# Kernel tuning notes

Measured on AMD Instinct MI355X. Metric: run time of the kernel, lower is better.

The kernel has to match this reference:

```python
import jax, jax.numpy as jnp
import numpy as np


def _gru_cell(x, h, Wih, Whh, bih, bhh):
    # torch nn.GRU cell math: gates ordered [r, z, n]
    gi = Wih @ x + bih
    gh = Whh @ h + bhh
    ir, iz, inn = jnp.split(gi, 3)
    hr, hz, hn = jnp.split(gh, 3)
    r = jax.nn.sigmoid(ir + hr)
    z = jax.nn.sigmoid(iz + hz)
    n = jnp.tanh(inn + r * hn)
    return (1.0 - z) * n + z * h


def _lrelu(x):
    # torch nn.LeakyReLU default negative_slope=0.01
    return jnp.where(x >= 0, x, 0.01 * x)


def setup_inputs() -> dict:
    key = jax.random.key(0)
    ks = jax.random.split(key, 24)
    V, E, H, C, S, T = 32000, 512, 1024, 2048, 256, 129
    w = lambda k, shape: jax.random.normal(k, shape, jnp.float32) * 0.02
    return {
        "inputs": jax.random.randint(ks[0], (T,), 0, V),
        "h1": jax.random.normal(ks[1], (H,), jnp.float32),
        "h2": jax.random.normal(ks[2], (H,), jnp.float32),
        "projected_keys": jax.random.normal(ks[3], (S, H), jnp.float32),
        "encoder_outputs": jax.random.normal(ks[4], (S, C), jnp.float32),
        "embeds": jax.random.normal(ks[5], (V, E), jnp.float32),
        "Wq": w(ks[6], (H, H)),
        "v_att": w(ks[7], (H,)),
        "W_ih1": w(ks[8], (3 * H, E + C)),
        "W_hh1": w(ks[9], (3 * H, H)),
        "b_ih1": w(ks[10], (3 * H,)),
        "b_hh1": w(ks[11], (3 * H,)),
        "W_ih2": w(ks[12], (3 * H, H + C)),
        "W_hh2": w(ks[13], (3 * H, H)),
        "b_ih2": w(ks[14], (3 * H,)),
        "b_hh2": w(ks[15], (3 * H,)),
        "W_pre": w(ks[16], (H, E + H + C)),
        "b_pre": w(ks[17], (H,)),
        "W_out": w(ks[18], (E, H)),
        "b_out": w(ks[19], (E,)),
    }


def reference(inputs, h1, h2, projected_keys, encoder_outputs, embeds, Wq, v_att,
              W_ih1, W_hh1, b_ih1, b_hh1, W_ih2, W_hh2, b_ih2, b_hh2,
              W_pre, b_pre, W_out, b_out):
    # teacher_forcing = 1.0 -> decoder input at step i is inputs[i] (ground truth)
    emb_seq = embeds[inputs[:-1]]  # [T-1, E]

    def step(carry, emb):
        h1, h2 = carry
        # additive attention: query from top-layer hidden state
        q = Wq @ h2                                     # [H]
        e = jnp.tanh(projected_keys + q) @ v_att        # [S]
        alphas = jax.nn.softmax(e)                      # [S]
        context = alphas @ encoder_outputs              # [C]
        h1n = _gru_cell(jnp.concatenate([emb, context]), h1, W_ih1, W_hh1, b_ih1, b_hh1)
        o1 = _lrelu(h1n)                                # dropout identity (eval)
        h2n = _gru_cell(jnp.concatenate([o1, context]), h2, W_ih2, W_hh2, b_ih2, b_hh2)
        o2 = _lrelu(h2n)
        pre = _lrelu(W_pre @ jnp.concatenate([emb, o2, context]) + b_pre)  # [H]
        out = W_out @ o2 + b_out                        # [E]
        return (h1n, h2n), (out, pre, alphas)

    (h1f, h2f), (outs, pres, alphas) = jax.lax.scan(step, (h1, h2), emb_seq)
    # torch.cat(outputs, dim=1) of [1,1,E] pieces -> [1, T-1, E]
    return outs[None], pres[None], alphas, h1f, h2f
```

## Files before the change

kernel.cpp:

```cpp
#include <hip/hip_runtime.h>

typedef unsigned int uint32;

#define GBLK 256
#define BT 512
#define NSTEP 128

struct Params {
  const int* inputs;
  const float *h1_in, *h2_in, *embeds, *vatt;
  const float *pk, *enc, *Wq, *Wih1, *Whh1, *Wih2, *Whh2, *Wpre, *Wout;
  const float *bih1, *bhh1, *bih2, *bhh2, *bpre, *bout;
  float* out;
  float* ws;
  int* bar;
};

__device__ __forceinline__ float blo(uint32 u) { return __uint_as_float(u << 16); }
__device__ __forceinline__ float bhi(uint32 u) { return __uint_as_float(u & 0xffff0000u); }
__device__ __forceinline__ uint32 bfr(float f) {
  uint32 u = __float_as_uint(f);
  return (u + 0x7fffu + ((u >> 16) & 1u)) >> 16;
}

__device__ __forceinline__ float ald(const float* a) {
  return __hip_atomic_load(a, __ATOMIC_RELAXED, __HIP_MEMORY_SCOPE_AGENT);
}
__device__ __forceinline__ void ast(float* a, float v) {
  __hip_atomic_store(a, v, __ATOMIC_RELAXED, __HIP_MEMORY_SCOPE_AGENT);
}

__device__ __forceinline__ float wsum(float v) {
#pragma unroll
  for (int o = 32; o; o >>= 1) v += __shfl_xor(v, o, 64);
  return v;
}

__device__ __forceinline__ void ldchunk(const float* W, size_t base, int lane, uint32* r) {
  const float* wf = W + base + lane * 8;
  float4 a = *(const float4*)wf;
  float4 c = *(const float4*)(wf + 4);
  r[0] = bfr(a.x) | (bfr(a.y) << 16);
  r[1] = bfr(a.z) | (bfr(a.w) << 16);
  r[2] = bfr(c.x) | (bfr(c.y) << 16);
  r[3] = bfr(c.z) | (bfr(c.w) << 16);
}

__device__ __forceinline__ float dotchunk(const uint32* r, const float* xc, int lane) {
  const float* x = xc + lane * 8;
  float4 x0 = *(const float4*)x, x1 = *(const float4*)(x + 4);
  return blo(r[0]) * x0.x + bhi(r[0]) * x0.y + blo(r[1]) * x0.z + bhi(r[1]) * x0.w +
         blo(r[2]) * x1.x + bhi(r[2]) * x1.y + blo(r[3]) * x1.z + bhi(r[3]) * x1.w;
}

__device__ __forceinline__ void gbar(int* bar, int k) {
  __syncthreads();
  if (threadIdx.x == 0) {
    const int grp = blockIdx.x >> 4;
    int* gcnt = bar + grp * 32;
    int* grel = bar + 512 + grp * 32;
    int* rcnt = bar + 1024;
    int* rrel = bar + 1056;
    int v = __hip_atomic_fetch_add(gcnt, 1, __ATOMIC_RELEASE, __HIP_MEMORY_SCOPE_AGENT);
    if (v == k * 16 - 1) {
      int r = __hip_atomic_fetch_add(rcnt, 1, __ATOMIC_RELEASE, __HIP_MEMORY_SCOPE_AGENT);
      if (r == k * 16 - 1)
        __hip_atomic_store(rrel, k, __ATOMIC_RELAXED, __HIP_MEMORY_SCOPE_AGENT);
      while (__hip_atomic_load(rrel, __ATOMIC_RELAXED, __HIP_MEMORY_SCOPE_AGENT) < k)
        __builtin_amdgcn_s_sleep(1);
      __hip_atomic_store(grel, k, __ATOMIC_RELAXED, __HIP_MEMORY_SCOPE_AGENT);
    } else {
      while (__hip_atomic_load(grel, __ATOMIC_RELAXED, __HIP_MEMORY_SCOPE_AGENT) < k)
        __builtin_amdgcn_s_sleep(1);
    }
  }
  __syncthreads();
}

__device__ __forceinline__ float sigm(float x) { return 1.f / (1.f + expf(-x)); }
__device__ __forceinline__ float lrelu(float x) { return x >= 0.f ? x : 0.01f * x; }

__global__ __launch_bounds__(BT, 2) void dec_regw_kernel(Params p) {
  __shared__ float sx[5632];
  __shared__ float s_red[8];
  __shared__ float s_part[72];

  const int tid = threadIdx.x;
  const int lane = tid & 63;
  const int w = tid >> 6;
  const int b = blockIdx.x;
  const int gw = b * 8 + w;
  const int i0 = b * 4;
  const int j0 = b * 8;

  float* h1w = p.ws + 2048;
  float* h2w = p.ws + 3072;
  float* qw = p.ws + 4096;
  float* evw = p.ws + 5120;
  float* ctxw = p.ws + 5376;
  float* o1w = p.ws + 7424;
  float* o2w = p.ws + 8448;
  float* gh1 = p.ws + 9472;
  float* gh2 = p.ws + 12544;

  float* outs = p.out;
  float* pres = p.out + 65536;
  float* alph = p.out + 196608;
  float* h1f = p.out + 229376;
  float* h2f = p.out + 230400;

  uint32 wa[48];
  if (gw < 1024) {
#pragma unroll
    for (int c = 0; c < 7; ++c)
      ldchunk(p.Wpre, (size_t)gw * 3584 + c * 512, lane, wa + 4 * c);
    ldchunk(p.Whh1, (size_t)gw * 1024, lane, wa + 28);
    ldchunk(p.Whh1, (size_t)gw * 1024 + 512, lane, wa + 32);
    ldchunk(p.Whh1, (size_t)(gw + 1024) * 1024, lane, wa + 36);
    ldchunk(p.Whh1, (size_t)(gw + 1024) * 1024 + 512, lane, wa + 40);
    wa[44] = wa[45] = wa[46] = wa[47] = 0u;
  } else {
    const int widx = gw - 1024;
    ldchunk(p.Whh1, (size_t)(2048 + widx) * 1024, lane, wa + 0);
    ldchunk(p.Whh1, (size_t)(2048 + widx) * 1024 + 512, lane, wa + 4);
#pragma unroll
    for (int r = 0; r < 3; ++r) {
      ldchunk(p.Whh2, (size_t)(widx + r * 1024) * 1024, lane, wa + 8 + 8 * r);
      ldchunk(p.Whh2, (size_t)(widx + r * 1024) * 1024 + 512, lane, wa + 12 + 8 * r);
    }
    ldchunk(p.Wq, (size_t)widx * 1024, lane, wa + 32);
    ldchunk(p.Wq, (size_t)widx * 1024 + 512, lane, wa + 36);
    const int wr = widx & 511;
    ldchunk(p.Wout, (size_t)wr * 1024, lane, wa + 40);
    ldchunk(p.Wout, (size_t)wr * 1024 + 512, lane, wa + 44);
  }

  uint32 wd[32];
#pragma unroll
  for (int k = 0; k < 8; ++k) {
    const int mm = w + 8 * k;
    const int mmc = mm < 60 ? mm : 0;
    const int r = mmc / 15, m = mmc % 15, g = m / 5, c = m % 5;
    ldchunk(p.Wih1, (size_t)(g * 1024 + i0 + r) * 2560 + c * 512, lane, wd + 4 * k);
  }

  uint32 we9[36];
#pragma unroll
  for (int k = 0; k < 9; ++k) {
    const int mm = w + 8 * k;
    const int r = mm / 18, m = mm % 18, g = m / 6, c = m % 6;
    ldchunk(p.Wih2, (size_t)(g * 1024 + i0 + r) * 3072 + c * 512, lane, we9 + 4 * k);
  }

  uint32 wenc[4] = {0u, 0u, 0u, 0u};
  if (tid < 256) {
    const float* er = p.enc + (size_t)tid * 2048 + j0;
    float4 a = *(const float4*)er, c = *(const float4*)(er + 4);
    wenc[0] = bfr(a.x) | (bfr(a.y) << 16);
    wenc[1] = bfr(a.z) | (bfr(a.w) << 16);
    wenc[2] = bfr(c.x) | (bfr(c.y) << 16);
    wenc[3] = bfr(c.z) | (bfr(c.w) << 16);
  }

  const int d0 = tid * 2;
  const float pk0 = p.pk[(size_t)b * 1024 + d0];
  const float pk1 = p.pk[(size_t)b * 1024 + d0 + 1];
  const float va0 = p.vatt[d0];
  const float va1 = p.vatt[d0 + 1];

  if (gw < 16) ast(h1w + gw * 64 + lane, p.h1_in[gw * 64 + lane]);
  else if (gw < 32) ast(h2w + (gw - 16) * 64 + lane, p.h2_in[(gw - 16) * 64 + lane]);

  int bk = 0;
  gbar(p.bar, ++bk);

  for (int t = 0; t <= NSTEP; ++t) {
    gbar(p.bar, ++bk);
    {
      const float* embp = p.embeds + (size_t)p.inputs[t > 0 ? t - 1 : 0] * 512;
      for (int i = tid; i < 5632; i += BT) {
        float v;
        if (i < 512) v = embp[i];
        else if (i < 1536) v = ald(o2w + i - 512);
        else if (i < 3584) v = ald(ctxw + i - 1536);
        else if (i < 4608) v = ald(h1w + i - 3584);
        else v = ald(h2w + i - 4608);
        sx[i] = v;
      }
      __syncthreads();
      if (gw < 1024) {
        if (t > 0) {
          float s = 0.f;
#pragma unroll
          for (int c = 0; c < 7; ++c) s += dotchunk(wa + 4 * c, sx + 512 * c, lane);
          s = wsum(s);
          if (lane == 0) pres[(size_t)(t - 1) * 1024 + gw] = lrelu(s + p.bpre[gw]);
        }
        float s1 = dotchunk(wa + 28, sx + 3584, lane) + dotchunk(wa + 32, sx + 4096, lane);
        s1 = wsum(s1);
        if (lane == 0) ast(gh1 + gw, s1 + p.bhh1[gw]);
        float s2 = dotchunk(wa + 36, sx + 3584, lane) + dotchunk(wa + 40, sx + 4096, lane);
        s2 = wsum(s2);
        if (lane == 0) ast(gh1 + 1024 + gw, s2 + p.bhh1[1024 + gw]);
      } else {
        const int widx = gw - 1024;
        float s = dotchunk(wa + 0, sx + 3584, lane) + dotchunk(wa + 4, sx + 4096, lane);
        s = wsum(s);
        if (lane == 0) ast(gh1 + 2048 + widx, s + p.bhh1[2048 + widx]);
#pragma unroll
        for (int r = 0; r < 3; ++r) {
          float t2 = dotchunk(wa + 8 + 8 * r, sx + 4608, lane) +
                     dotchunk(wa + 12 + 8 * r, sx + 5120, lane);
          t2 = wsum(t2);
          if (lane == 0) ast(gh2 + widx + 1024 * r, t2 + p.bhh2[widx + 1024 * r]);
        }
        float sq = dotchunk(wa + 32, sx + 4608, lane) + dotchunk(wa + 36, sx + 5120, lane);
        sq = wsum(sq);
        if (lane == 0) ast(qw + widx, sq);
        if (t > 0 && widx < 512) {
          float so = dotchunk(wa + 40, sx + 512, lane) + dotchunk(wa + 44, sx + 1024, lane);
          so = wsum(so);
          if (lane == 0) outs[(size_t)(t - 1) * 512 + widx] = so + p.bout[widx];
        }
      }
    }
    if (t == NSTEP) break;

    gbar(p.bar, ++bk);
    {
      float q0 = ald(qw + d0), q1 = ald(qw + d0 + 1);
      float acc = va0 * tanhf(pk0 + q0) + va1 * tanhf(pk1 + q1);
      acc = wsum(acc);
      if (lane == 0) s_red[w] = acc;
      __syncthreads();
      if (tid == 0) {
        float e = s_red[0] + s_red[1] + s_red[2] + s_red[3] +
                  s_red[4] + s_red[5] + s_red[6] + s_red[7];
        ast(evw + b, e);
      }
    }

    gbar(p.bar, ++bk);
    {
      float e_i = 0.f, pe = 0.f;
      if (tid < 256) {
        e_i = ald(evw + tid);
        float mw = e_i;
#pragma unroll
        for (int o = 32; o; o >>= 1) mw = fmaxf(mw, __shfl_xor(mw, o, 64));
        if (lane == 0) s_red[w] = mw;
      }
      __syncthreads();
      float m = fmaxf(fmaxf(s_red[0], s_red[1]), fmaxf(s_red[2], s_red[3]));
      __syncthreads();
      if (tid < 256) {
        pe = expf(e_i - m);
        float zw = wsum(pe);
        if (lane == 0) s_red[w] = zw;
      }
      __syncthreads();
      float Z = s_red[0] + s_red[1] + s_red[2] + s_red[3];
      if (tid < 256) {
        float alpha = pe / Z;
        if (b == 0) alph[(size_t)t * 256 + tid] = alpha;
        sx[tid * 8 + 0] = alpha * blo(wenc[0]);
        sx[tid * 8 + 1] = alpha * bhi(wenc[0]);
        sx[tid * 8 + 2] = alpha * blo(wenc[1]);
        sx[tid * 8 + 3] = alpha * bhi(wenc[1]);
        sx[tid * 8 + 4] = alpha * blo(wenc[2]);
        sx[tid * 8 + 5] = alpha * bhi(wenc[2]);
        sx[tid * 8 + 6] = alpha * blo(wenc[3]);
        sx[tid * 8 + 7] = alpha * bhi(wenc[3]);
      }
      __syncthreads();
      for (int st = 128; st >= 1; st >>= 1) {
        if (tid < st) {
#pragma unroll
          for (int j = 0; j < 8; ++j) sx[tid * 8 + j] += sx[(tid + st) * 8 + j];
        }
        __syncthreads();
      }
      if (tid < 8) ast(ctxw + j0 + tid, sx[tid]);
    }

    gbar(p.bar, ++bk);
    {
      const float* embc = p.embeds + (size_t)p.inputs[t] * 512;
      for (int i = tid; i < 2560; i += BT)
        sx[i] = (i < 512) ? embc[i] : ald(ctxw + i - 512);
      __syncthreads();
#pragma unroll
      for (int k = 0; k < 8; ++k) {
        const int mm = w + 8 * k;
        if (mm < 60) {
          const int c = (mm % 15) % 5;
          float s = dotchunk(wd + 4 * k, sx + c * 512, lane);
          s = wsum(s);
          if (lane == 0) s_part[mm] = s;
        }
      }
      __syncthreads();
      if (tid < 4) {
        const int i = i0 + tid;
        const float* sp = s_part + tid * 15;
        float sr = sp[0] + sp[1] + sp[2] + sp[3] + sp[4];
        float sz = sp[5] + sp[6] + sp[7] + sp[8] + sp[9];
        float sn = sp[10] + sp[11] + sp[12] + sp[13] + sp[14];
        float r = sigm(sr + p.bih1[i] + ald(gh1 + i));
        float z = sigm(sz + p.bih1[1024 + i] + ald(gh1 + 1024 + i));
        float n = tanhf(sn + p.bih1[2048 + i] + r * ald(gh1 + 2048 + i));
        float h = (1.f - z) * n + z * ald(h1w + i);
        ast(h1w + i, h);
        ast(o1w + i, lrelu(h));
      }
    }

    gbar(p.bar, ++bk);
    {
      for (int i = tid; i < 3072; i += BT)
        sx[i] = (i < 1024) ? ald(o1w + i) : ald(ctxw + i - 1024);
      __syncthreads();
#pragma unroll
      for (int k = 0; k < 9; ++k) {
        const int mm = w + 8 * k;
        const int c = (mm % 18) % 6;
        float s = dotchunk(we9 + 4 * k, sx + c * 512, lane);
        s = wsum(s);
        if (lane == 0) s_part[mm] = s;
      }
      __syncthreads();
      if (tid < 4) {
        const int i = i0 + tid;
        const float* sp = s_part + tid * 18;
        float sr = sp[0] + sp[1] + sp[2] + sp[3] + sp[4] + sp[5];
        float sz = sp[6] + sp[7] + sp[8] + sp[9] + sp[10] + sp[11];
        float sn = sp[12] + sp[13] + sp[14] + sp[15] + sp[16] + sp[17];
        float r = sigm(sr + p.bih2[i] + ald(gh2 + i));
        float z = sigm(sz + p.bih2[1024 + i] + ald(gh2 + 1024 + i));
        float n = tanhf(sn + p.bih2[2048 + i] + r * ald(gh2 + 2048 + i));
        float h = (1.f - z) * n + z * ald(h2w + i);
        ast(h2w + i, h);
        ast(o2w + i, lrelu(h));
      }
    }
  }
  if (gw < 16) h1f[gw * 64 + lane] = ald(h1w + gw * 64 + lane);
  else if (gw < 32) h2f[(gw - 16) * 64 + lane] = ald(h2w + (gw - 16) * 64 + lane);
}

extern "C" void kernel_launch(void* const* d_in, const int* in_sizes, int n_in,
                              void* d_out, int out_size, void* d_ws, size_t ws_size,
                              hipStream_t stream) {
  hipMemsetAsync(d_ws, 0, 65536, stream);

  Params p;
  p.inputs = (const int*)d_in[0];
  p.h1_in = (const float*)d_in[1];
  p.h2_in = (const float*)d_in[2];
  p.pk = (const float*)d_in[3];
  p.enc = (const float*)d_in[4];
  p.embeds = (const float*)d_in[5];
  p.Wq = (const float*)d_in[6];
  p.vatt = (const float*)d_in[7];
  p.Wih1 = (const float*)d_in[8];
  p.Whh1 = (const float*)d_in[9];
  p.bih1 = (const float*)d_in[10];
  p.bhh1 = (const float*)d_in[11];
  p.Wih2 = (const float*)d_in[12];
  p.Whh2 = (const float*)d_in[13];
  p.bih2 = (const float*)d_in[14];
  p.bhh2 = (const float*)d_in[15];
  p.Wpre = (const float*)d_in[16];
  p.bpre = (const float*)d_in[17];
  p.Wout = (const float*)d_in[18];
  p.bout = (const float*)d_in[19];
  p.out = (float*)d_out;
  p.ws = (float*)d_ws;
  p.bar = (int*)d_ws;

  void* args[] = {&p};
  hipError_t err = hipLaunchCooperativeKernel((const void*)dec_regw_kernel,
                                              dim3(GBLK), dim3(BT), args, 0, stream);
  if (err != hipSuccess) {
    dec_regw_kernel<<<dim3(GBLK), dim3(BT), 0, stream>>>(p);
  }
}
```

Baseline: 7.239 ms.

## Replace grid barriers with epoch-tagged 64-bit dataflow flags per value

Removes the hierarchical grid barrier and instead packs each shared workspace value with an epoch tag in a 64-bit word. Consumers spin until the tags they need reach the current step, so stages can overlap: the pre/out projection for the previous step now runs off the critical path after the recurrent hidden-state matvecs. The context reduction moves from a shared-memory tree to wave shuffles. The trade-off is more polling traffic on many 64-bit atomics and wider workspace loads, plus ordering that relies on relaxed atomics rather than explicit fences.

Result: faster. 6.434 ms (-11.1%).

```diff
diff --git a/kernel.cpp b/kernel.cpp
--- a/kernel.cpp
+++ b/kernel.cpp
@@ -1,10 +1,21 @@
 #include <hip/hip_runtime.h>
 
 typedef unsigned int uint32;
+typedef unsigned long long u64;
 
 #define GBLK 256
 #define BT 512
 #define NSTEP 128
+
+#define QE    0
+#define EE    1024
+#define CTXE  1280
+#define H1E   3328
+#define H2E   4352
+#define O1E   5376
+#define O2E   6400
+#define GH1E  7424
+#define GH2E  10496
 
 struct Params {
   const int* inputs;
@@ -13,7 +24,6 @@
   const float *bih1, *bhh1, *bih2, *bhh2, *bpre, *bout;
   float* out;
   float* ws;
-  int* bar;
 };
 
 __device__ __forceinline__ float blo(uint32 u) { return __uint_as_float(u << 16); }
@@ -23,12 +33,17 @@
   return (u + 0x7fffu + ((u >> 16) & 1u)) >> 16;
 }
 
-__device__ __forceinline__ float ald(const float* a) {
+__device__ __forceinline__ u64 ald64(const u64* a) {
   return __hip_atomic_load(a, __ATOMIC_RELAXED, __HIP_MEMORY_SCOPE_AGENT);
 }
-__device__ __forceinline__ void ast(float* a, float v) {
+__device__ __forceinline__ void ast64(u64* a, u64 v) {
   __hip_atomic_store(a, v, __ATOMIC_RELAXED, __HIP_MEMORY_SCOPE_AGENT);
 }
+__device__ __forceinline__ u64 pk64(float f, uint32 ep) {
+  return ((u64)ep << 32) | (u64)__float_as_uint(f);
+}
+__device__ __forceinline__ float lo32f(u64 v) { return __uint_as_float((uint32)v); }
+__device__ __forceinline__ bool tok(u64 v, uint32 tg) { return (uint32)(v >> 32) >= tg; }
 
 __device__ __forceinline__ float wsum(float v) {
 #pragma unroll
@@ -53,35 +68,11 @@
          blo(r[2]) * x1.x + bhi(r[2]) * x1.y + blo(r[3]) * x1.z + bhi(r[3]) * x1.w;
 }
 
-__device__ __forceinline__ void gbar(int* bar, int k) {
-  __syncthreads();
-  if (threadIdx.x == 0) {
-    const int grp = blockIdx.x >> 4;
-    int* gcnt = bar + grp * 32;
-    int* grel = bar + 512 + grp * 32;
-    int* rcnt = bar + 1024;
-    int* rrel = bar + 1056;
-    int v = __hip_atomic_fetch_add(gcnt, 1, __ATOMIC_RELEASE, __HIP_MEMORY_SCOPE_AGENT);
-    if (v == k * 16 - 1) {
-      int r = __hip_atomic_fetch_add(rcnt, 1, __ATOMIC_RELEASE, __HIP_MEMORY_SCOPE_AGENT);
-      if (r == k * 16 - 1)
-        __hip_atomic_store(rrel, k, __ATOMIC_RELAXED, __HIP_MEMORY_SCOPE_AGENT);
-      while (__hip_atomic_load(rrel, __ATOMIC_RELAXED, __HIP_MEMORY_SCOPE_AGENT) < k)
-        __builtin_amdgcn_s_sleep(1);
-      __hip_atomic_store(grel, k, __ATOMIC_RELAXED, __HIP_MEMORY_SCOPE_AGENT);
-    } else {
-      while (__hip_atomic_load(grel, __ATOMIC_RELAXED, __HIP_MEMORY_SCOPE_AGENT) < k)
-        __builtin_amdgcn_s_sleep(1);
-    }
-  }
-  __syncthreads();
-}
-
 __device__ __forceinline__ float sigm(float x) { return 1.f / (1.f + expf(-x)); }
 __device__ __forceinline__ float lrelu(float x) { return x >= 0.f ? x : 0.01f * x; }
 
-__global__ __launch_bounds__(BT, 2) void dec_regw_kernel(Params p) {
-  __shared__ float sx[5632];
+__global__ __launch_bounds__(BT, 2) void dec_flow_kernel(Params p) {
+  __shared__ float sx[8192];
   __shared__ float s_red[8];
   __shared__ float s_part[72];
 
@@ -93,15 +84,7 @@
   const int i0 = b * 4;
   const int j0 = b * 8;
 
-  float* h1w = p.ws + 2048;
-  float* h2w = p.ws + 3072;
-  float* qw = p.ws + 4096;
-  float* evw = p.ws + 5120;
-  float* ctxw = p.ws + 5376;
-  float* o1w = p.ws + 7424;
-  float* o2w = p.ws + 8448;
-  float* gh1 = p.ws + 9472;
-  float* gh2 = p.ws + 12544;
+  u64* wsu = (u64*)p.ws;
 
   float* outs = p.out;
   float* pres = p.out + 65536;
@@ -168,67 +151,100 @@
   const float va0 = p.vatt[d0];
   const float va1 = p.vatt[d0 + 1];
 
-  if (gw < 16) ast(h1w + gw * 64 + lane, p.h1_in[gw * 64 + lane]);
-  else if (gw < 32) ast(h2w + (gw - 16) * 64 + lane, p.h2_in[(gw - 16) * 64 + lane]);
-
-  int bk = 0;
-  gbar(p.bar, ++bk);
+  if (gw < 16) ast64(wsu + H1E + gw * 64 + lane, pk64(p.h1_in[gw * 64 + lane], 1));
+  else if (gw < 32) ast64(wsu + H2E + (gw - 16) * 64 + lane, pk64(p.h2_in[(gw - 16) * 64 + lane], 1));
 
   for (int t = 0; t <= NSTEP; ++t) {
-    gbar(p.bar, ++bk);
+    const uint32 TP = (uint32)(t + 1);
+    const uint32 TS = (uint32)(t + 2);
+
+    if (t < NSTEP) {
+      {
+        const u64 *a0 = wsu + H1E + tid, *a1 = wsu + H1E + 512 + tid;
+        const u64 *a2 = wsu + H2E + tid, *a3 = wsu + H2E + 512 + tid;
+        u64 v0, v1, v2, v3;
+        for (;;) {
+          v0 = ald64(a0); v1 = ald64(a1); v2 = ald64(a2); v3 = ald64(a3);
+          if (tok(v0, TP) && tok(v1, TP) && tok(v2, TP) && tok(v3, TP)) break;
+          __builtin_amdgcn_s_sleep(1);
+        }
+        sx[6144 + tid] = lo32f(v0); sx[6656 + tid] = lo32f(v1);
+        sx[7168 + tid] = lo32f(v2); sx[7680 + tid] = lo32f(v3);
+      }
+      __syncthreads();
+      if (gw >= 1024) {
+        const int widx = gw - 1024;
+        float sq = dotchunk(wa + 32, sx + 7168, lane) + dotchunk(wa + 36, sx + 7680, lane);
+        sq = wsum(sq);
+        if (lane == 0) ast64(wsu + QE + widx, pk64(sq, TS));
+        float s = dotchunk(wa + 0, sx + 6144, lane) + dotchunk(wa + 4, sx + 6656, lane);
+        s = wsum(s);
+        if (lane == 0) ast64(wsu + GH1E + 2048 + widx, pk64(s + p.bhh1[2048 + widx], TS));
+#pragma unroll
+        for (int r = 0; r < 3; ++r) {
+          float t2 = dotchunk(wa + 8 + 8 * r, sx + 7168, lane) +
+                     dotchunk(wa + 12 + 8 * r, sx + 7680, lane);
+          t2 = wsum(t2);
+          if (lane == 0) ast64(wsu + GH2E + widx + 1024 * r, pk64(t2 + p.bhh2[widx + 1024 * r], TS));
+        }
+      } else {
+        float s1 = dotchunk(wa + 28, sx + 6144, lane) + dotchunk(wa + 32, sx + 6656, lane);
+        s1 = wsum(s1);
+        if (lane == 0) ast64(wsu + GH1E + gw, pk64(s1 + p.bhh1[gw], TS));
+        float s2 = dotchunk(wa + 36, sx + 6144, lane) + dotchunk(wa + 40, sx + 6656, lane);
+        s2 = wsum(s2);
+        if (lane == 0) ast64(wsu + GH1E + 1024 + gw, pk64(s2 + p.bhh1[1024 + gw], TS));
+      }
+    }
+
+    if (t > 0) {
+      {
+        const float* embp = p.embeds + (size_t)p.inputs[t - 1] * 512;
+        float ev = embp[tid];
+        const u64 *a0 = wsu + O2E + tid, *a1 = wsu + O2E + 512 + tid;
+        const u64 *c0 = wsu + CTXE + tid, *c1 = wsu + CTXE + 512 + tid;
+        const u64 *c2 = wsu + CTXE + 1024 + tid, *c3 = wsu + CTXE + 1536 + tid;
+        u64 v0, v1, u0, u1, u2, u3;
+        for (;;) {
+          v0 = ald64(a0); v1 = ald64(a1);
+          u0 = ald64(c0); u1 = ald64(c1); u2 = ald64(c2); u3 = ald64(c3);
+          if (tok(v0, TP) && tok(v1, TP) && tok(u0, TP) && tok(u1, TP) &&
+              tok(u2, TP) && tok(u3, TP)) break;
+          __builtin_amdgcn_s_sleep(1);
+        }
+        sx[tid] = ev;
+        sx[512 + tid] = lo32f(v0); sx[1024 + tid] = lo32f(v1);
+        sx[1536 + tid] = lo32f(u0); sx[2048 + tid] = lo32f(u1);
+        sx[2560 + tid] = lo32f(u2); sx[3072 + tid] = lo32f(u3);
+      }
+      __syncthreads();
+      if (gw < 1024) {
+        float s = 0.f;
+#pragma unroll
+        for (int c = 0; c < 7; ++c) s += dotchunk(wa + 4 * c, sx + 512 * c, lane);
+        s = wsum(s);
+        if (lane == 0) pres[(size_t)(t - 1) * 1024 + gw] = lrelu(s + p.bpre[gw]);
+      } else if (gw - 1024 < 512) {
+        const int widx = gw - 1024;
+        float so = dotchunk(wa + 40, sx + 512, lane) + dotchunk(wa + 44, sx + 1024, lane);
+        so = wsum(so);
+        if (lane == 0) outs[(size_t)(t - 1) * 512 + widx] = so + p.bout[widx];
+      }
+    }
+    if (t == NSTEP) break;
+
     {
-      const float* embp = p.embeds + (size_t)p.inputs[t > 0 ? t - 1 : 0] * 512;
-      for (int i = tid; i < 5632; i += BT) {
-        float v;
-        if (i < 512) v = embp[i];
-        else if (i < 1536) v = ald(o2w + i - 512);
-        else if (i < 3584) v = ald(ctxw + i - 1536);
-        else if (i < 4608) v = ald(h1w + i - 3584);
-        else v = ald(h2w + i - 4608);
-        sx[i] = v;
-      }
-      __syncthreads();
-      if (gw < 1024) {
-        if (t > 0) {
-          float s = 0.f;
-#pragma unroll
-          for (int c = 0; c < 7; ++c) s += dotchunk(wa + 4 * c, sx + 512 * c, lane);
-          s = wsum(s);
-          if (lane == 0) pres[(size_t)(t - 1) * 1024 + gw] = lrelu(s + p.bpre[gw]);
-        }
-        float s1 = dotchunk(wa + 28, sx + 3584, lane) + dotchunk(wa + 32, sx + 4096, lane);
-        s1 = wsum(s1);
-        if (lane == 0) ast(gh1 + gw, s1 + p.bhh1[gw]);
-        float s2 = dotchunk(wa + 36, sx + 3584, lane) + dotchunk(wa + 40, sx + 4096, lane);
-        s2 = wsum(s2);
-        if (lane == 0) ast(gh1 + 1024 + gw, s2 + p.bhh1[1024 + gw]);
-      } else {
-        const int widx = gw - 1024;
-        float s = dotchunk(wa + 0, sx + 3584, lane) + dotchunk(wa + 4, sx + 4096, lane);
-        s = wsum(s);
-        if (lane == 0) ast(gh1 + 2048 + widx, s + p.bhh1[2048 + widx]);
-#pragma unroll
-        for (int r = 0; r < 3; ++r) {
-          float t2 = dotchunk(wa + 8 + 8 * r, sx + 4608, lane) +
-                     dotchunk(wa + 12 + 8 * r, sx + 5120, lane);
-          t2 = wsum(t2);
-          if (lane == 0) ast(gh2 + widx + 1024 * r, t2 + p.bhh2[widx + 1024 * r]);
-        }
-        float sq = dotchunk(wa + 32, sx + 4608, lane) + dotchunk(wa + 36, sx + 5120, lane);
-        sq = wsum(sq);
-        if (lane == 0) ast(qw + widx, sq);
-        if (t > 0 && widx < 512) {
-          float so = dotchunk(wa + 40, sx + 512, lane) + dotchunk(wa + 44, sx + 1024, lane);
-          so = wsum(so);
-          if (lane == 0) outs[(size_t)(t - 1) * 512 + widx] = so + p.bout[widx];
-        }
-      }
-    }
-    if (t == NSTEP) break;
-
-    gbar(p.bar, ++bk);
-    {
-      float q0 = ald(qw + d0), q1 = ald(qw + d0 + 1);
+      float q0, q1;
+      {
+        const u64 *a0 = wsu + QE + d0, *a1 = wsu + QE + d0 + 1;
+        u64 v0, v1;
+        for (;;) {
+          v0 = ald64(a0); v1 = ald64(a1);
+          if (tok(v0, TS) && tok(v1, TS)) break;
+          __builtin_amdgcn_s_sleep(1);
+        }
+        q0 = lo32f(v0); q1 = lo32f(v1);
+      }
       float acc = va0 * tanhf(pk0 + q0) + va1 * tanhf(pk1 + q1);
       acc = wsum(acc);
       if (lane == 0) s_red[w] = acc;
@@ -236,15 +252,14 @@
       if (tid == 0) {
         float e = s_red[0] + s_red[1] + s_red[2] + s_red[3] +
                   s_red[4] + s_red[5] + s_red[6] + s_red[7];
-        ast(evw + b, e);
-      }
-    }
-
-    gbar(p.bar, ++bk);
-    {
+        ast64(wsu + EE + b, pk64(e, TS));
+      }
+      __syncthreads();
       float e_i = 0.f, pe = 0.f;
       if (tid < 256) {
-        e_i = ald(evw + tid);
+        u64 v = ald64(wsu + EE + tid);
+        while (!tok(v, TS)) { __builtin_amdgcn_s_sleep(1); v = ald64(wsu + EE + tid); }
+        e_i = lo32f(v);
         float mw = e_i;
 #pragma unroll
         for (int o = 32; o; o >>= 1) mw = fmaxf(mw, __shfl_xor(mw, o, 64));
@@ -263,31 +278,57 @@
       if (tid < 256) {
         float alpha = pe / Z;
         if (b == 0) alph[(size_t)t * 256 + tid] = alpha;
-        sx[tid * 8 + 0] = alpha * blo(wenc[0]);
-        sx[tid * 8 + 1] = alpha * bhi(wenc[0]);
-        sx[tid * 8 + 2] = alpha * blo(wenc[1]);
-        sx[tid * 8 + 3] = alpha * bhi(wenc[1]);
-        sx[tid * 8 + 4] = alpha * blo(wenc[2]);
-        sx[tid * 8 + 5] = alpha * bhi(wenc[2]);
-        sx[tid * 8 + 6] = alpha * blo(wenc[3]);
-        sx[tid * 8 + 7] = alpha * bhi(wenc[3]);
-      }
-      __syncthreads();
-      for (int st = 128; st >= 1; st >>= 1) {
-        if (tid < st) {
-#pragma unroll
-          for (int j = 0; j < 8; ++j) sx[tid * 8 + j] += sx[(tid + st) * 8 + j];
-        }
-        __syncthreads();
-      }
-      if (tid < 8) ast(ctxw + j0 + tid, sx[tid]);
-    }
-
-    gbar(p.bar, ++bk);
+        float c[8];
+        c[0] = alpha * blo(wenc[0]); c[1] = alpha * bhi(wenc[0]);
+        c[2] = alpha * blo(wenc[1]); c[3] = alpha * bhi(wenc[1]);
+        c[4] = alpha * blo(wenc[2]); c[5] = alpha * bhi(wenc[2]);
+        c[6] = alpha * blo(wenc[3]); c[7] = alpha * bhi(wenc[3]);
+#pragma unroll
+        for (int o = 32; o; o >>= 1) {
+#pragma unroll
+          for (int j = 0; j < 8; ++j) c[j] += __shfl_xor(c[j], o, 64);
+        }
+        if (lane == 0) {
+#pragma unroll
+          for (int j = 0; j < 8; ++j) s_part[w * 8 + j] = c[j];
+        }
+      }
+      __syncthreads();
+      if (tid < 8) {
+        float cj = s_part[tid] + s_part[8 + tid] + s_part[16 + tid] + s_part[24 + tid];
+        ast64(wsu + CTXE + j0 + tid, pk64(cj, TS));
+      }
+    }
+
     {
-      const float* embc = p.embeds + (size_t)p.inputs[t] * 512;
-      for (int i = tid; i < 2560; i += BT)
-        sx[i] = (i < 512) ? embc[i] : ald(ctxw + i - 512);
+      float g1a = 0.f, g1b = 0.f, g1c = 0.f, h1old = 0.f;
+      if (tid < 4) {
+        const int i = i0 + tid;
+        u64 x0, x1, x2;
+        for (;;) {
+          x0 = ald64(wsu + GH1E + i); x1 = ald64(wsu + GH1E + 1024 + i);
+          x2 = ald64(wsu + GH1E + 2048 + i);
+          if (tok(x0, TS) && tok(x1, TS) && tok(x2, TS)) break;
+          __builtin_amdgcn_s_sleep(1);
+        }
+        g1a = lo32f(x0); g1b = lo32f(x1); g1c = lo32f(x2);
+        h1old = sx[6144 + i];
+      }
+      {
+        const float* embc = p.embeds + (size_t)p.inputs[t] * 512;
+        float ev = embc[tid];
+        const u64 *c0 = wsu + CTXE + tid, *c1 = wsu + CTXE + 512 + tid;
+        const u64 *c2 = wsu + CTXE + 1024 + tid, *c3 = wsu + CTXE + 1536 + tid;
+        u64 u0, u1, u2, u3;
+        for (;;) {
+          u0 = ald64(c0); u1 = ald64(c1); u2 = ald64(c2); u3 = ald64(c3);
+          if (tok(u0, TS) && tok(u1, TS) && tok(u2, TS) && tok(u3, TS)) break;
+          __builtin_amdgcn_s_sleep(1);
+        }
+        sx[tid] = ev;
+        sx[512 + tid] = lo32f(u0); sx[1024 + tid] = lo32f(u1);
+        sx[1536 + tid] = lo32f(u2); sx[2048 + tid] = lo32f(u3);
+      }
       __syncthreads();
 #pragma unroll
       for (int k = 0; k < 8; ++k) {
@@ -306,25 +347,46 @@
         float sr = sp[0] + sp[1] + sp[2] + sp[3] + sp[4];
         float sz = sp[5] + sp[6] + sp[7] + sp[8] + sp[9];
         float sn = sp[10] + sp[11] + sp[12] + sp[13] + sp[14];
-        float r = sigm(sr + p.bih1[i] + ald(gh1 + i));
-        float z = sigm(sz + p.bih1[1024 + i] + ald(gh1 + 1024 + i));
-        float n = tanhf(sn + p.bih1[2048 + i] + r * ald(gh1 + 2048 + i));
-        float h = (1.f - z) * n + z * ald(h1w + i);
-        ast(h1w + i, h);
-        ast(o1w + i, lrelu(h));
-      }
-    }
-
-    gbar(p.bar, ++bk);
+        float r = sigm(sr + p.bih1[i] + g1a);
+        float z = sigm(sz + p.bih1[1024 + i] + g1b);
+        float n = tanhf(sn + p.bih1[2048 + i] + r * g1c);
+        float h = (1.f - z) * n + z * h1old;
+        ast64(wsu + H1E + i, pk64(h, TS));
+        ast64(wsu + O1E + i, pk64(lrelu(h), TS));
+      }
+    }
+
     {
-      for (int i = tid; i < 3072; i += BT)
-        sx[i] = (i < 1024) ? ald(o1w + i) : ald(ctxw + i - 1024);
+      float g2a = 0.f, g2b = 0.f, g2c = 0.f, h2old = 0.f;
+      if (tid < 4) {
+        const int i = i0 + tid;
+        u64 x0, x1, x2;
+        for (;;) {
+          x0 = ald64(wsu + GH2E + i); x1 = ald64(wsu + GH2E + 1024 + i);
+          x2 = ald64(wsu + GH2E + 2048 + i);
+          if (tok(x0, TS) && tok(x1, TS) && tok(x2, TS)) break;
+          __builtin_amdgcn_s_sleep(1);
+        }
+        g2a = lo32f(x0); g2b = lo32f(x1); g2c = lo32f(x2);
+        h2old = sx[7168 + i];
+      }
+      {
+        const u64 *a0 = wsu + O1E + tid, *a1 = wsu + O1E + 512 + tid;
+        u64 v0, v1;
+        for (;;) {
+          v0 = ald64(a0); v1 = ald64(a1);
+          if (tok(v0, TS) && tok(v1, TS)) break;
+          __builtin_amdgcn_s_sleep(1);
+        }
+        sx[2560 + tid] = lo32f(v0); sx[3072 + tid] = lo32f(v1);
+      }
       __syncthreads();
 #pragma unroll
       for (int k = 0; k < 9; ++k) {
         const int mm = w + 8 * k;
         const int c = (mm % 18) % 6;
-        float s = dotchunk(we9 + 4 * k, sx + c * 512, lane);
+        const float* xp = (c < 2) ? (sx + 2560 + c * 512) : (sx + 512 + (c - 2) * 512);
+        float s = dotchunk(we9 + 4 * k, xp, lane);
         s = wsum(s);
         if (lane == 0) s_part[mm] = s;
       }
@@ -335,23 +397,31 @@
         float sr = sp[0] + sp[1] + sp[2] + sp[3] + sp[4] + sp[5];
         float sz = sp[6] + sp[7] + sp[8] + sp[9] + sp[10] + sp[11];
         float sn = sp[12] + sp[13] + sp[14] + sp[15] + sp[16] + sp[17];
-        float r = sigm(sr + p.bih2[i] + ald(gh2 + i));
-        float z = sigm(sz + p.bih2[1024 + i] + ald(gh2 + 1024 + i));
-        float n = tanhf(sn + p.bih2[2048 + i] + r * ald(gh2 + 2048 + i));
-        float h = (1.f - z) * n + z * ald(h2w + i);
-        ast(h2w + i, h);
-        ast(o2w + i, lrelu(h));
-      }
-    }
-  }
-  if (gw < 16) h1f[gw * 64 + lane] = ald(h1w + gw * 64 + lane);
-  else if (gw < 32) h2f[(gw - 16) * 64 + lane] = ald(h2w + (gw - 16) * 64 + lane);
+        float r = sigm(sr + p.bih2[i] + g2a);
+        float z = sigm(sz + p.bih2[1024 + i] + g2b);
+        float n = tanhf(sn + p.bih2[2048 + i] + r * g2c);
+        float h = (1.f - z) * n + z * h2old;
+        ast64(wsu + H2E + i, pk64(h, TS));
+        ast64(wsu + O2E + i, pk64(lrelu(h), TS));
+      }
+    }
+  }
+
+  if (gw < 16) {
+    u64 v = ald64(wsu + H1E + gw * 64 + lane);
+    while (!tok(v, NSTEP + 1)) { __builtin_amdgcn_s_sleep(1); v = ald64(wsu + H1E + gw * 64 + lane); }
+    h1f[gw * 64 + lane] = lo32f(v);
+  } else if (gw < 32) {
+    u64 v = ald64(wsu + H2E + (gw - 16) * 64 + lane);
+    while (!tok(v, NSTEP + 1)) { __builtin_amdgcn_s_sleep(1); v = ald64(wsu + H2E + (gw - 16) * 64 + lane); }
+    h2f[(gw - 16) * 64 + lane] = lo32f(v);
+  }
 }
 
 extern "C" void kernel_launch(void* const* d_in, const int* in_sizes, int n_in,
                               void* d_out, int out_size, void* d_ws, size_t ws_size,
                               hipStream_t stream) {
-  hipMemsetAsync(d_ws, 0, 65536, stream);
+  hipMemsetAsync(d_ws, 0, 131072, stream);
 
   Params p;
   p.inputs = (const int*)d_in[0];
@@ -376,12 +446,11 @@
   p.bout = (const float*)d_in[19];
   p.out = (float*)d_out;
   p.ws = (float*)d_ws;
-  p.bar = (int*)d_ws;
 
   void* args[] = {&p};
-  hipError_t err = hipLaunchCooperativeKernel((const void*)dec_regw_kernel,
+  hipError_t err = hipLaunchCooperativeKernel((const void*)dec_flow_kernel,
                                               dim3(GBLK), dim3(BT), args, 0, stream);
   if (err != hipSuccess) {
-    dec_regw_kernel<<<dim3(GBLK), dim3(BT), 0, stream>>>(p);
-  }
-}
+    dec_flow_kernel<<<dim3(GBLK), dim3(BT), 0, stream>>>(p);
+  }
+}
```
